# Kernel tuning notes

Measured on AMD Instinct MI355X. Metric: run time of the kernel, lower is better.

Reference implementation:

```python
import jax, jax.numpy as jnp
import numpy as np

N_NODES = 20000
N_EDGES = 320000
HIDDEN = 256
N_GRAPHS = 64
IN_DIM = 3
OUT_DIM = 2


def _glorot(key, shape):
    fan_in, fan_out = shape
    lim = jnp.sqrt(6.0 / (fan_in + fan_out))
    return jax.random.uniform(key, shape, jnp.float32, -lim, lim)


def setup_inputs() -> dict:
    key = jax.random.key(0)
    ks = jax.random.split(key, 16)
    inp = {
        "x": jax.random.normal(ks[0], (N_NODES, IN_DIM), jnp.float32),
        "edge_index": jax.random.randint(ks[1], (2, N_EDGES), 0, N_NODES, jnp.int64),
        "batch": jnp.sort(jax.random.randint(ks[2], (N_NODES,), 0, N_GRAPHS, jnp.int64)),
        "W1": _glorot(ks[3], (IN_DIM, HIDDEN)), "b1": jnp.zeros((HIDDEN,), jnp.float32),
        "W2": _glorot(ks[4], (HIDDEN, HIDDEN)), "b2": jnp.zeros((HIDDEN,), jnp.float32),
        "W3": _glorot(ks[5], (HIDDEN, HIDDEN)), "b3": jnp.zeros((HIDDEN,), jnp.float32),
        "W4": _glorot(ks[6], (HIDDEN, HIDDEN)), "b4": jnp.zeros((HIDDEN,), jnp.float32),
        "W5": _glorot(ks[7], (HIDDEN, HIDDEN)), "b5": jnp.zeros((HIDDEN,), jnp.float32),
        "Wlin": _glorot(ks[8], (HIDDEN, OUT_DIM)), "blin": jnp.zeros((OUT_DIM,), jnp.float32),
    }
    return inp


def _gcn_norm(edge_index, n_nodes):
    # PyG GCNConv default: add self-loops, symmetric degree normalization.
    loops = jnp.arange(n_nodes, dtype=edge_index.dtype)
    src = jnp.concatenate([edge_index[0], loops])
    dst = jnp.concatenate([edge_index[1], loops])
    deg = jax.ops.segment_sum(jnp.ones_like(dst, jnp.float32), dst, num_segments=n_nodes)
    dinv = jnp.where(deg > 0, jax.lax.rsqrt(deg), 0.0)
    norm = dinv[src] * dinv[dst]  # [E + N]
    return src, dst, norm


def _gcn_layer(x, W, b, src, dst, norm, n_nodes):
    h = x @ W                                   # [N, H]
    msg = h[src] * norm[:, None]                # [E+N, H] gather + scale
    agg = jax.ops.segment_sum(msg, dst, num_segments=n_nodes)  # scatter-add
    return agg + b


def reference(x, edge_index, batch, W1, b1, W2, b2, W3, b3, W4, b4, W5, b5, Wlin, blin):
    n = x.shape[0]
    src, dst, norm = _gcn_norm(edge_index, n)
    h = jax.nn.relu(_gcn_layer(x, W1, b1, src, dst, norm, n))
    h = jax.nn.relu(_gcn_layer(h, W2, b2, src, dst, norm, n))
    h = jax.nn.relu(_gcn_layer(h, W3, b3, src, dst, norm, n))
    h = jax.nn.relu(_gcn_layer(h, W4, b4, src, dst, norm, n))
    h = jax.nn.relu(_gcn_layer(h, W5, b5, src, dst, norm, n))
    pooled = jax.ops.segment_sum(h, batch, num_segments=N_GRAPHS)  # global_add_pool
    return pooled @ Wlin + blin
```

## Files before the change

### kernel.cpp

```cpp
#include <hip/hip_runtime.h>

#define N_NODES 20000
#define N_PAD 20096
#define N_EDGES 320000
#define HIDDEN 256
#define N_GRAPHS 64
#define OUT_DIM 2

#define QPANEL_BYTES 65536
#define QTABLE_BYTES 32768
#define GEMM_GRID 628
#define ECACHE 1536

typedef __attribute__((ext_vector_type(8))) short short8v;
typedef __attribute__((ext_vector_type(4))) float f32x4;
typedef __attribute__((ext_vector_type(4))) unsigned short us4;

__global__ void k_zero(int* __restrict__ degi, float* __restrict__ pooled) {
    int i = blockIdx.x * 256 + threadIdx.x;
    if (i < N_NODES) degi[i] = 0;
    if (i < N_GRAPHS * HIDDEN) pooled[i] = 0.f;
}

__global__ void k_degree_wprep(const int* __restrict__ dst, int* __restrict__ degi,
                               const float* __restrict__ W2, const float* __restrict__ W3,
                               const float* __restrict__ W4, const float* __restrict__ W5,
                               char* __restrict__ wt) {
    int bid = blockIdx.x;
    if (bid < 1250) {
        int e = bid * 256 + threadIdx.x;
        if (e < N_EDGES) atomicAdd(&degi[dst[e]], 1);
        return;
    }
    int wb = bid - 1250;
    int lid = wb >> 8;
    int idx = (wb & 255) * 256 + threadIdx.x;
    const float* W = lid == 0 ? W2 : lid == 1 ? W3 : lid == 2 ? W4 : W5;
    int k = idx & 255, n = idx >> 8;
    float a = W[k * 256 + n];
    unsigned u = __float_as_uint(a);
    ushort hi = (ushort)(u >> 16);
    float hif = __uint_as_float(u & 0xffff0000u);
    ushort lo = (ushort)(__float_as_uint(a - hif) >> 16);
    int q = n >> 6, colQ = n & 63, slab = k >> 3, e = k & 7;
    size_t base = ((size_t)lid * 4 + q) * QPANEL_BYTES;
    size_t soff = (size_t)slab * 1024 + ((colQ * 16 + slab * 32) & 1023) + e * 2;
    *(ushort*)(wt + base + soff) = hi;
    *(ushort*)(wt + base + QTABLE_BYTES + soff) = lo;
}

__global__ void k_scan(const int* __restrict__ degi, int* __restrict__ rowptr,
                       int* __restrict__ rowstart, float* __restrict__ dinv) {
    __shared__ int sums[1024];
    int t = threadIdx.x;
    int base = t * 20;
    int ld[20];
    int local = 0;
    if (t < 1000) {
#pragma unroll
        for (int i = 0; i < 20; ++i) {
            ld[i] = degi[base + i];
            local += ld[i];
            dinv[base + i] = rsqrtf((float)ld[i] + 1.0f);
        }
    }
    sums[t] = local;
    __syncthreads();
    for (int off = 1; off < 1024; off <<= 1) {
        int v = (t >= off) ? sums[t - off] : 0;
        __syncthreads();
        sums[t] += v;
        __syncthreads();
    }
    if (t < 1000) {
        int run = (t == 0) ? 0 : sums[t - 1];
#pragma unroll
        for (int i = 0; i < 20; ++i) {
            rowptr[base + i] = run;
            rowstart[base + i] = run;
            run += ld[i];
        }
    }
    if (t == 1023) rowptr[N_NODES] = sums[1023];
}

__global__ void k_fill(const int* __restrict__ src, const int* __restrict__ dst,
                       const float* __restrict__ dinv, int* __restrict__ rowstart,
                       int2* __restrict__ csr) {
    int e = blockIdx.x * blockDim.x + threadIdx.x;
    if (e >= N_EDGES) return;
    int s = src[e], d = dst[e];
    int pos = atomicAdd(&rowstart[d], 1);
    csr[pos] = make_int2(s, __float_as_int(dinv[s] * dinv[d]));
}

__global__ void k_aggx(const float* __restrict__ x, const float* __restrict__ dinv,
                       const int* __restrict__ rowptr, const int2* __restrict__ csr,
                       float* __restrict__ z) {
    int t = blockIdx.x * blockDim.x + threadIdx.x;
    int i = t >> 2, c = t & 3;
    if (i >= N_NODES || c >= 3) return;
    float di = dinv[i];
    float a = di * di * x[i * 3 + c], bacc = 0.f;
    int k = rowptr[i], end = rowptr[i + 1];
    for (; k + 1 < end; k += 2) {
        int2 e0 = csr[k], e1 = csr[k + 1];
        a = fmaf(x[(size_t)e0.x * 3 + c], __int_as_float(e0.y), a);
        bacc = fmaf(x[(size_t)e1.x * 3 + c], __int_as_float(e1.y), bacc);
    }
    if (k < end) {
        int2 e0 = csr[k];
        a = fmaf(x[(size_t)e0.x * 3 + c], __int_as_float(e0.y), a);
    }
    z[i * 3 + c] = a + bacc;
}

__global__ void k_h1(const float* __restrict__ z, const float* __restrict__ W1,
                     const float* __restrict__ b1,
                     ushort* __restrict__ out_hi, ushort* __restrict__ out_lo) {
    int i = blockIdx.x;
    int j = threadIdx.x;
    float z0 = z[i * 3], z1 = z[i * 3 + 1], z2 = z[i * 3 + 2];
    float v = fmaf(z0, W1[j], fmaf(z1, W1[256 + j], fmaf(z2, W1[512 + j], b1[j])));
    v = fmaxf(v, 0.0f);
    unsigned u = __float_as_uint(v);
    ushort hi = (ushort)(u >> 16);
    float hif = __uint_as_float(u & 0xffff0000u);
    ushort lo = (ushort)(__float_as_uint(v - hif) >> 16);
    out_hi[(size_t)i * HIDDEN + j] = hi;
    out_lo[(size_t)i * HIDDEN + j] = lo;
}

__global__ void k_csr_agg(const float* __restrict__ h, const float* __restrict__ dinv,
                          const int* __restrict__ rowptr, const int2* __restrict__ csr,
                          const float* __restrict__ b,
                          ushort* __restrict__ out_hi, ushort* __restrict__ out_lo) {
    __shared__ int2 ec[ECACHE];
    int bid = blockIdx.x;
    int slice = bid & 7;
    int nodeBase = (bid >> 3) * 32;
    int begB = rowptr[nodeBase];
    int total = rowptr[nodeBase + 32] - begB;
    bool cached = (total <= ECACHE);
    if (cached) {
        for (int i = threadIdx.x; i < total; i += 256) ec[i] = csr[begB + i];
        __syncthreads();
    }
    int node = nodeBase + (threadIdx.x >> 3);
    int cl = threadIdx.x & 7;
    int scol = slice * 32 + cl * 4;
    int beg = rowptr[node] - begB, end = rowptr[node + 1] - begB;
    const int2* ep = cached ? ec : (csr + begB);
    float4 A0 = {0,0,0,0}, A1 = {0,0,0,0}, A2 = {0,0,0,0}, A3 = {0,0,0,0};
    int k = beg;
    for (; k + 3 < end; k += 4) {
        int2 e0 = ep[k], e1 = ep[k + 1], e2 = ep[k + 2], e3 = ep[k + 3];
        float w0 = __int_as_float(e0.y), w1 = __int_as_float(e1.y);
        float w2 = __int_as_float(e2.y), w3 = __int_as_float(e3.y);
        float4 v0 = *reinterpret_cast<const float4*>(h + (size_t)e0.x * HIDDEN + scol);
        float4 v1 = *reinterpret_cast<const float4*>(h + (size_t)e1.x * HIDDEN + scol);
        float4 v2 = *reinterpret_cast<const float4*>(h + (size_t)e2.x * HIDDEN + scol);
        float4 v3 = *reinterpret_cast<const float4*>(h + (size_t)e3.x * HIDDEN + scol);
        A0.x = fmaf(v0.x, w0, A0.x);  A1.x = fmaf(v1.x, w1, A1.x);
        A0.y = fmaf(v0.y, w0, A0.y);  A1.y = fmaf(v1.y, w1, A1.y);
        A0.z = fmaf(v0.z, w0, A0.z);  A1.z = fmaf(v1.z, w1, A1.z);
        A0.w = fmaf(v0.w, w0, A0.w);  A1.w = fmaf(v1.w, w1, A1.w);
        A2.x = fmaf(v2.x, w2, A2.x);  A3.x = fmaf(v3.x, w3, A3.x);
        A2.y = fmaf(v2.y, w2, A2.y);  A3.y = fmaf(v3.y, w3, A3.y);
        A2.z = fmaf(v2.z, w2, A2.z);  A3.z = fmaf(v3.z, w3, A3.z);
        A2.w = fmaf(v2.w, w2, A2.w);  A3.w = fmaf(v3.w, w3, A3.w);
    }
    if (k + 1 < end) {
        int2 e0 = ep[k], e1 = ep[k + 1];
        float w0 = __int_as_float(e0.y), w1 = __int_as_float(e1.y);
        float4 v0 = *reinterpret_cast<const float4*>(h + (size_t)e0.x * HIDDEN + scol);
        float4 v1 = *reinterpret_cast<const float4*>(h + (size_t)e1.x * HIDDEN + scol);
        A0.x = fmaf(v0.x, w0, A0.x);  A1.x = fmaf(v1.x, w1, A1.x);
        A0.y = fmaf(v0.y, w0, A0.y);  A1.y = fmaf(v1.y, w1, A1.y);
        A0.z = fmaf(v0.z, w0, A0.z);  A1.z = fmaf(v1.z, w1, A1.z);
        A0.w = fmaf(v0.w, w0, A0.w);  A1.w = fmaf(v1.w, w1, A1.w);
        k += 2;
    }
    if (k < end) {
        int2 e0 = ep[k];
        float w0 = __int_as_float(e0.y);
        float4 v0 = *reinterpret_cast<const float4*>(h + (size_t)e0.x * HIDDEN + scol);
        A0.x = fmaf(v0.x, w0, A0.x);
        A0.y = fmaf(v0.y, w0, A0.y);
        A0.z = fmaf(v0.z, w0, A0.z);
        A0.w = fmaf(v0.w, w0, A0.w);
    }
    float di = dinv[node];
    float ws = di * di;
    float4 bv = *reinterpret_cast<const float4*>(b + scol);
    float4 hv = *reinterpret_cast<const float4*>(h + (size_t)node * HIDDEN + scol);
    float rv[4];
    rv[0] = fmaxf(fmaf(hv.x, ws, bv.x + (A0.x + A1.x) + (A2.x + A3.x)), 0.f);
    rv[1] = fmaxf(fmaf(hv.y, ws, bv.y + (A0.y + A1.y) + (A2.y + A3.y)), 0.f);
    rv[2] = fmaxf(fmaf(hv.z, ws, bv.z + (A0.z + A1.z) + (A2.z + A3.z)), 0.f);
    rv[3] = fmaxf(fmaf(hv.w, ws, bv.w + (A0.w + A1.w) + (A2.w + A3.w)), 0.f);
    us4 hvv, lvv;
#pragma unroll
    for (int j = 0; j < 4; ++j) {
        unsigned u = __float_as_uint(rv[j]);
        hvv[j] = (ushort)(u >> 16);
        float hif = __uint_as_float(u & 0xffff0000u);
        lvv[j] = (ushort)(__float_as_uint(rv[j] - hif) >> 16);
    }
    *reinterpret_cast<us4*>(out_hi + (size_t)node * HIDDEN + scol) = hvv;
    *reinterpret_cast<us4*>(out_lo + (size_t)node * HIDDEN + scol) = lvv;
}

__global__ __launch_bounds__(512) void k_gemm_mfma(const ushort* __restrict__ a_hi,
                                                   const ushort* __restrict__ a_lo,
                                                   const char* __restrict__ wpanels,
                                                   float* __restrict__ out) {
    __shared__ char smem[QPANEL_BYTES];
    int d = blockIdx.x;
    int xcd = d & 7, idx = d >> 3;
    const int q0 = GEMM_GRID / 8, r = GEMM_GRID % 8;
    int base = xcd * q0 + (xcd < r ? xcd : r);
    int logical = base + idx;
    int mtile = logical >> 2, q = logical & 3;

    const char* gsrc = wpanels + (size_t)q * QPANEL_BYTES;
    int tid = threadIdx.x;
#pragma unroll
    for (int it = 0; it < 8; ++it) {
        int o = it * 8192 + tid * 16;
        *reinterpret_cast<float4*>(smem + o) = *reinterpret_cast<const float4*>(gsrc + o);
    }
    __syncthreads();

    int w = tid >> 6, l = tid & 63;
    int lr = l & 15, kg = l >> 4;
    int wm = w >> 1, wn = w & 1;
    int row0 = mtile * 128 + wm * 32;
    int colQ0 = wn * 32;

    const ushort* aph = a_hi + (size_t)(row0 + lr) * HIDDEN + kg * 8;
    const ushort* apl = a_lo + (size_t)(row0 + lr) * HIDDEN + kg * 8;

    short8v ah0 = *reinterpret_cast<const short8v*>(aph);
    short8v ah1 = *reinterpret_cast<const short8v*>(aph + 16 * HIDDEN);
    short8v al0 = *reinterpret_cast<const short8v*>(apl);
    short8v al1 = *reinterpret_cast<const short8v*>(apl + 16 * HIDDEN);

    f32x4 acc[2][2] = {};
#pragma unroll
    for (int t = 0; t < 8; ++t) {
        short8v cah0 = ah0, cah1 = ah1, cal0 = al0, cal1 = al1;
        if (t < 7) {
            int kb = (t + 1) * 32;
            ah0 = *reinterpret_cast<const short8v*>(aph + kb);
            ah1 = *reinterpret_cast<const short8v*>(aph + 16 * HIDDEN + kb);
            al0 = *reinterpret_cast<const short8v*>(apl + kb);
            al1 = *reinterpret_cast<const short8v*>(apl + 16 * HIDDEN + kb);
        }
        int slab = t * 4 + kg;
        int sbase = slab * 1024;
        int rot = slab * 32;
        int off0 = sbase + (((colQ0 + lr) * 16 + rot) & 1023);
        int off1 = sbase + (((colQ0 + 16 + lr) * 16 + rot) & 1023);
        short8v bh0 = *reinterpret_cast<const short8v*>(smem + off0);
        short8v bh1 = *reinterpret_cast<const short8v*>(smem + off1);
        short8v bl0 = *reinterpret_cast<const short8v*>(smem + QTABLE_BYTES + off0);
        short8v bl1 = *reinterpret_cast<const short8v*>(smem + QTABLE_BYTES + off1);
        acc[0][0] = __builtin_amdgcn_mfma_f32_16x16x32_bf16(cah0, bh0, acc[0][0], 0, 0, 0);
        acc[1][0] = __builtin_amdgcn_mfma_f32_16x16x32_bf16(cah1, bh0, acc[1][0], 0, 0, 0);
        acc[0][1] = __builtin_amdgcn_mfma_f32_16x16x32_bf16(cah0, bh1, acc[0][1], 0, 0, 0);
        acc[1][1] = __builtin_amdgcn_mfma_f32_16x16x32_bf16(cah1, bh1, acc[1][1], 0, 0, 0);
        acc[0][0] = __builtin_amdgcn_mfma_f32_16x16x32_bf16(cal0, bh0, acc[0][0], 0, 0, 0);
        acc[1][0] = __builtin_amdgcn_mfma_f32_16x16x32_bf16(cal1, bh0, acc[1][0], 0, 0, 0);
        acc[0][1] = __builtin_amdgcn_mfma_f32_16x16x32_bf16(cal0, bh1, acc[0][1], 0, 0, 0);
        acc[1][1] = __builtin_amdgcn_mfma_f32_16x16x32_bf16(cal1, bh1, acc[1][1], 0, 0, 0);
        acc[0][0] = __builtin_amdgcn_mfma_f32_16x16x32_bf16(cah0, bl0, acc[0][0], 0, 0, 0);
        acc[1][0] = __builtin_amdgcn_mfma_f32_16x16x32_bf16(cah1, bl0, acc[1][0], 0, 0, 0);
        acc[0][1] = __builtin_amdgcn_mfma_f32_16x16x32_bf16(cah0, bl1, acc[0][1], 0, 0, 0);
        acc[1][1] = __builtin_amdgcn_mfma_f32_16x16x32_bf16(cah1, bl1, acc[1][1], 0, 0, 0);
    }
    int gcol = q * 64 + colQ0 + lr;
#pragma unroll
    for (int rf = 0; rf < 2; ++rf) {
        float* o0 = out + (size_t)(row0 + rf * 16 + kg * 4) * HIDDEN + gcol;
#pragma unroll
        for (int rr = 0; rr < 4; ++rr)
#pragma unroll
            for (int cf = 0; cf < 2; ++cf)
                o0[(size_t)rr * HIDDEN + cf * 16] = acc[rf][cf][rr];
    }
}

__global__ void k_pool(const ushort* __restrict__ hi, const ushort* __restrict__ lo,
                       const int* __restrict__ batch, float* __restrict__ pooled) {
    int base = blockIdx.x * 32;
    int j = threadIdx.x;
    float acc = 0.0f;
    int cur = batch[base];
    for (int r = 0; r < 32; ++r) {
        int i = base + r;
        int bg = batch[i];
        if (bg != cur) {
            atomicAdd(&pooled[cur * HIDDEN + j], acc);
            acc = 0.0f;
            cur = bg;
        }
        size_t off = (size_t)i * HIDDEN + j;
        float v = __uint_as_float((unsigned)hi[off] << 16) +
                  __uint_as_float((unsigned)lo[off] << 16);
        acc += v;
    }
    atomicAdd(&pooled[cur * HIDDEN + j], acc);
}

__global__ void k_final(const float* __restrict__ pooled, const float* __restrict__ Wlin,
                        const float* __restrict__ blin, float* __restrict__ out) {
    int t = threadIdx.x;
    int g = t >> 1, o = t & 1;
    float s = blin[o];
    for (int k = 0; k < HIDDEN; ++k) s += pooled[g * HIDDEN + k] * Wlin[k * OUT_DIM + o];
    out[g * OUT_DIM + o] = s;
}

extern "C" void kernel_launch(void* const* d_in, const int* in_sizes, int n_in,
                              void* d_out, int out_size, void* d_ws, size_t ws_size,
                              hipStream_t stream) {
    const float* x     = (const float*)d_in[0];
    const int*   esrc  = (const int*)d_in[1];
    const int*   edst  = esrc + N_EDGES;
    const int*   batch = (const int*)d_in[2];
    const float* W1 = (const float*)d_in[3];
    const float* b1 = (const float*)d_in[4];
    const float* W2 = (const float*)d_in[5];
    const float* b2 = (const float*)d_in[6];
    const float* W3 = (const float*)d_in[7];
    const float* b3 = (const float*)d_in[8];
    const float* W4 = (const float*)d_in[9];
    const float* b4 = (const float*)d_in[10];
    const float* W5 = (const float*)d_in[11];
    const float* b5 = (const float*)d_in[12];
    const float* Wlin = (const float*)d_in[13];
    const float* blin = (const float*)d_in[14];
    float* out = (float*)d_out;

    char* ws = (char*)d_ws;
    size_t off = 0;
    auto alloc = [&](size_t bytes) { size_t o = off; off += (bytes + 255) & ~size_t(255); return (void*)(ws + o); };

    int*    degi     = (int*)alloc(N_NODES * 4);
    float*  dinv     = (float*)alloc(N_NODES * 4);
    int*    rowptr   = (int*)alloc((N_NODES + 1) * 4);
    int*    rowstart = (int*)alloc(N_NODES * 4);
    int2*   csr      = (int2*)alloc((size_t)N_EDGES * 8);
    float*  hA       = (float*)alloc((size_t)N_PAD * HIDDEN * 4);
    ushort* hb_hi    = (ushort*)alloc((size_t)N_PAD * HIDDEN * 2);
    ushort* hb_lo    = (ushort*)alloc((size_t)N_PAD * HIDDEN * 2);
    float*  pooled   = (float*)alloc(N_GRAPHS * HIDDEN * 4);
    char*   wt       = (char*)alloc((size_t)4 * 4 * QPANEL_BYTES);
    float*  z        = (float*)alloc((size_t)N_NODES * 3 * 4);

    k_zero<<<(N_NODES + 255) / 256, 256, 0, stream>>>(degi, pooled);
    k_degree_wprep<<<1250 + 1024, 256, 0, stream>>>(edst, degi, W2, W3, W4, W5, wt);
    k_scan<<<1, 1024, 0, stream>>>(degi, rowptr, rowstart, dinv);
    k_fill<<<(N_EDGES + 255) / 256, 256, 0, stream>>>(esrc, edst, dinv, rowstart, csr);

    const float* bs[5] = {b1, b2, b3, b4, b5};

    k_aggx<<<(N_NODES * 4 + 255) / 256, 256, 0, stream>>>(x, dinv, rowptr, csr, z);
    k_h1<<<N_NODES, HIDDEN, 0, stream>>>(z, W1, b1, hb_hi, hb_lo);

    for (int l = 1; l < 5; ++l) {
        k_gemm_mfma<<<GEMM_GRID, 512, 0, stream>>>(
            hb_hi, hb_lo, wt + (size_t)(l - 1) * 4 * QPANEL_BYTES, hA);
        k_csr_agg<<<(N_NODES / 32) * 8, 256, 0, stream>>>(
            hA, dinv, rowptr, csr, bs[l], hb_hi, hb_lo);
    }

    k_pool<<<N_NODES / 32, HIDDEN, 0, stream>>>(hb_hi, hb_lo, batch, pooled);
    k_final<<<1, 128, 0, stream>>>(pooled, Wlin, blin, out);
}
```

Measured before the change: 341.9 us.

## Fuse first-layer aggregation with W1 projection and stream low weight panel from global

Merges the feature aggregation and first-layer projection kernels into one, keeping the aggregated 3-wide features in shared memory so the intermediate buffer and one launch disappear. Each block now handles 64 nodes and loops over them to write the bf16 hi/lo outputs. Separately, the MFMA GEMM now stages only the high-half weight panel in LDS and reads the low-half weight fragments directly from global memory with one-step prefetch, which halves LDS use and the per-block staging copy. The cost is extra global/L2 traffic for the low panel inside the inner loop.

```diff
diff --git a/kernel.cpp b/kernel.cpp
--- a/kernel.cpp
+++ b/kernel.cpp
@@ -94,41 +94,44 @@
     csr[pos] = make_int2(s, __float_as_int(dinv[s] * dinv[d]));
 }
 
-__global__ void k_aggx(const float* __restrict__ x, const float* __restrict__ dinv,
-                       const int* __restrict__ rowptr, const int2* __restrict__ csr,
-                       float* __restrict__ z) {
-    int t = blockIdx.x * blockDim.x + threadIdx.x;
-    int i = t >> 2, c = t & 3;
-    if (i >= N_NODES || c >= 3) return;
-    float di = dinv[i];
-    float a = di * di * x[i * 3 + c], bacc = 0.f;
-    int k = rowptr[i], end = rowptr[i + 1];
-    for (; k + 1 < end; k += 2) {
-        int2 e0 = csr[k], e1 = csr[k + 1];
-        a = fmaf(x[(size_t)e0.x * 3 + c], __int_as_float(e0.y), a);
-        bacc = fmaf(x[(size_t)e1.x * 3 + c], __int_as_float(e1.y), bacc);
-    }
-    if (k < end) {
-        int2 e0 = csr[k];
-        a = fmaf(x[(size_t)e0.x * 3 + c], __int_as_float(e0.y), a);
-    }
-    z[i * 3 + c] = a + bacc;
-}
-
-__global__ void k_h1(const float* __restrict__ z, const float* __restrict__ W1,
-                     const float* __restrict__ b1,
-                     ushort* __restrict__ out_hi, ushort* __restrict__ out_lo) {
-    int i = blockIdx.x;
-    int j = threadIdx.x;
-    float z0 = z[i * 3], z1 = z[i * 3 + 1], z2 = z[i * 3 + 2];
-    float v = fmaf(z0, W1[j], fmaf(z1, W1[256 + j], fmaf(z2, W1[512 + j], b1[j])));
-    v = fmaxf(v, 0.0f);
-    unsigned u = __float_as_uint(v);
-    ushort hi = (ushort)(u >> 16);
-    float hif = __uint_as_float(u & 0xffff0000u);
-    ushort lo = (ushort)(__float_as_uint(v - hif) >> 16);
-    out_hi[(size_t)i * HIDDEN + j] = hi;
-    out_lo[(size_t)i * HIDDEN + j] = lo;
+__global__ void k_aggx_h1(const float* __restrict__ x, const float* __restrict__ dinv,
+                          const int* __restrict__ rowptr, const int2* __restrict__ csr,
+                          const float* __restrict__ W1, const float* __restrict__ b1,
+                          ushort* __restrict__ out_hi, ushort* __restrict__ out_lo) {
+    __shared__ float zsh[64][4];
+    int base = blockIdx.x * 64;
+    int t = threadIdx.x;
+    int i = base + (t >> 2), c = t & 3;
+    if (i < N_NODES && c < 3) {
+        float di = dinv[i];
+        float a = di * di * x[i * 3 + c], bacc = 0.f;
+        int k = rowptr[i], end = rowptr[i + 1];
+        for (; k + 1 < end; k += 2) {
+            int2 e0 = csr[k], e1 = csr[k + 1];
+            a = fmaf(x[(size_t)e0.x * 3 + c], __int_as_float(e0.y), a);
+            bacc = fmaf(x[(size_t)e1.x * 3 + c], __int_as_float(e1.y), bacc);
+        }
+        if (k < end) {
+            int2 e0 = csr[k];
+            a = fmaf(x[(size_t)e0.x * 3 + c], __int_as_float(e0.y), a);
+        }
+        zsh[t >> 2][c] = a + bacc;
+    }
+    __syncthreads();
+    int j = t;
+    float w0 = W1[j], w1 = W1[256 + j], w2 = W1[512 + j], bb = b1[j];
+    int nmax = min(64, N_NODES - base);
+    for (int r = 0; r < nmax; ++r) {
+        float v = fmaf(zsh[r][0], w0, fmaf(zsh[r][1], w1, fmaf(zsh[r][2], w2, bb)));
+        v = fmaxf(v, 0.0f);
+        unsigned u = __float_as_uint(v);
+        ushort hi = (ushort)(u >> 16);
+        float hif = __uint_as_float(u & 0xffff0000u);
+        ushort lo = (ushort)(__float_as_uint(v - hif) >> 16);
+        size_t off = (size_t)(base + r) * HIDDEN + j;
+        out_hi[off] = hi;
+        out_lo[off] = lo;
+    }
 }
 
 __global__ void k_csr_agg(const float* __restrict__ h, const float* __restrict__ dinv,
@@ -215,7 +218,7 @@
                                                    const ushort* __restrict__ a_lo,
                                                    const char* __restrict__ wpanels,
                                                    float* __restrict__ out) {
-    __shared__ char smem[QPANEL_BYTES];
+    __shared__ char smem[QTABLE_BYTES];
     int d = blockIdx.x;
     int xcd = d & 7, idx = d >> 3;
     const int q0 = GEMM_GRID / 8, r = GEMM_GRID % 8;
@@ -224,9 +227,10 @@
     int mtile = logical >> 2, q = logical & 3;
 
     const char* gsrc = wpanels + (size_t)q * QPANEL_BYTES;
+    const char* glo = gsrc + QTABLE_BYTES;
     int tid = threadIdx.x;
 #pragma unroll
-    for (int it = 0; it < 8; ++it) {
+    for (int it = 0; it < 4; ++it) {
         int o = it * 8192 + tid * 16;
         *reinterpret_cast<float4*>(smem + o) = *reinterpret_cast<const float4*>(gsrc + o);
     }
@@ -241,31 +245,36 @@
     const ushort* aph = a_hi + (size_t)(row0 + lr) * HIDDEN + kg * 8;
     const ushort* apl = a_lo + (size_t)(row0 + lr) * HIDDEN + kg * 8;
 
+    auto boff = [&](int t, int colp) {
+        int slab = t * 4 + kg;
+        return slab * 1024 + (((colp + lr) * 16 + slab * 32) & 1023);
+    };
+
     short8v ah0 = *reinterpret_cast<const short8v*>(aph);
     short8v ah1 = *reinterpret_cast<const short8v*>(aph + 16 * HIDDEN);
     short8v al0 = *reinterpret_cast<const short8v*>(apl);
     short8v al1 = *reinterpret_cast<const short8v*>(apl + 16 * HIDDEN);
+    short8v bl0 = *reinterpret_cast<const short8v*>(glo + boff(0, colQ0));
+    short8v bl1 = *reinterpret_cast<const short8v*>(glo + boff(0, colQ0 + 16));
 
     f32x4 acc[2][2] = {};
 #pragma unroll
     for (int t = 0; t < 8; ++t) {
         short8v cah0 = ah0, cah1 = ah1, cal0 = al0, cal1 = al1;
+        short8v cbl0 = bl0, cbl1 = bl1;
         if (t < 7) {
             int kb = (t + 1) * 32;
             ah0 = *reinterpret_cast<const short8v*>(aph + kb);
             ah1 = *reinterpret_cast<const short8v*>(aph + 16 * HIDDEN + kb);
             al0 = *reinterpret_cast<const short8v*>(apl + kb);
             al1 = *reinterpret_cast<const short8v*>(apl + 16 * HIDDEN + kb);
-        }
-        int slab = t * 4 + kg;
-        int sbase = slab * 1024;
-        int rot = slab * 32;
-        int off0 = sbase + (((colQ0 + lr) * 16 + rot) & 1023);
-        int off1 = sbase + (((colQ0 + 16 + lr) * 16 + rot) & 1023);
+            bl0 = *reinterpret_cast<const short8v*>(glo + boff(t + 1, colQ0));
+            bl1 = *reinterpret_cast<const short8v*>(glo + boff(t + 1, colQ0 + 16));
+        }
+        int off0 = boff(t, colQ0);
+        int off1 = boff(t, colQ0 + 16);
         short8v bh0 = *reinterpret_cast<const short8v*>(smem + off0);
         short8v bh1 = *reinterpret_cast<const short8v*>(smem + off1);
-        short8v bl0 = *reinterpret_cast<const short8v*>(smem + QTABLE_BYTES + off0);
-        short8v bl1 = *reinterpret_cast<const short8v*>(smem + QTABLE_BYTES + off1);
         acc[0][0] = __builtin_amdgcn_mfma_f32_16x16x32_bf16(cah0, bh0, acc[0][0], 0, 0, 0);
         acc[1][0] = __builtin_amdgcn_mfma_f32_16x16x32_bf16(cah1, bh0, acc[1][0], 0, 0, 0);
         acc[0][1] = __builtin_amdgcn_mfma_f32_16x16x32_bf16(cah0, bh1, acc[0][1], 0, 0, 0);
@@ -274,10 +283,10 @@
         acc[1][0] = __builtin_amdgcn_mfma_f32_16x16x32_bf16(cal1, bh0, acc[1][0], 0, 0, 0);
         acc[0][1] = __builtin_amdgcn_mfma_f32_16x16x32_bf16(cal0, bh1, acc[0][1], 0, 0, 0);
         acc[1][1] = __builtin_amdgcn_mfma_f32_16x16x32_bf16(cal1, bh1, acc[1][1], 0, 0, 0);
-        acc[0][0] = __builtin_amdgcn_mfma_f32_16x16x32_bf16(cah0, bl0, acc[0][0], 0, 0, 0);
-        acc[1][0] = __builtin_amdgcn_mfma_f32_16x16x32_bf16(cah1, bl0, acc[1][0], 0, 0, 0);
-        acc[0][1] = __builtin_amdgcn_mfma_f32_16x16x32_bf16(cah0, bl1, acc[0][1], 0, 0, 0);
-        acc[1][1] = __builtin_amdgcn_mfma_f32_16x16x32_bf16(cah1, bl1, acc[1][1], 0, 0, 0);
+        acc[0][0] = __builtin_amdgcn_mfma_f32_16x16x32_bf16(cah0, cbl0, acc[0][0], 0, 0, 0);
+        acc[1][0] = __builtin_amdgcn_mfma_f32_16x16x32_bf16(cah1, cbl0, acc[1][0], 0, 0, 0);
+        acc[0][1] = __builtin_amdgcn_mfma_f32_16x16x32_bf16(cah0, cbl1, acc[0][1], 0, 0, 0);
+        acc[1][1] = __builtin_amdgcn_mfma_f32_16x16x32_bf16(cah1, cbl1, acc[1][1], 0, 0, 0);
     }
     int gcol = q * 64 + colQ0 + lr;
 #pragma unroll
@@ -357,7 +366,6 @@
     ushort* hb_lo    = (ushort*)alloc((size_t)N_PAD * HIDDEN * 2);
     float*  pooled   = (float*)alloc(N_GRAPHS * HIDDEN * 4);
     char*   wt       = (char*)alloc((size_t)4 * 4 * QPANEL_BYTES);
-    float*  z        = (float*)alloc((size_t)N_NODES * 3 * 4);
 
     k_zero<<<(N_NODES + 255) / 256, 256, 0, stream>>>(degi, pooled);
     k_degree_wprep<<<1250 + 1024, 256, 0, stream>>>(edst, degi, W2, W3, W4, W5, wt);
@@ -366,8 +374,8 @@
 
     const float* bs[5] = {b1, b2, b3, b4, b5};
 
-    k_aggx<<<(N_NODES * 4 + 255) / 256, 256, 0, stream>>>(x, dinv, rowptr, csr, z);
-    k_h1<<<N_NODES, HIDDEN, 0, stream>>>(z, W1, b1, hb_hi, hb_lo);
+    k_aggx_h1<<<(N_NODES + 63) / 64, 256, 0, stream>>>(x, dinv, rowptr, csr, W1, b1,
+                                                       hb_hi, hb_lo);
 
     for (int l = 1; l < 5; ++l) {
         k_gemm_mfma<<<GEMM_GRID, 512, 0, stream>>>(
```

Measured after the change: 345.9 us. Within noise of the previous version (+1.2%).
